# Kernel tuning notes

Hardware: AMD Instinct MI355X
Metric: run time of the kernel (lower is better)

The kernel has to match this reference:

```python
import jax, jax.numpy as jnp
import numpy as np

H = 128        # num_hidden
NIN = 384      # num_in
FF = 4 * H
SCALE = 30.0
EPS = 1e-5


def _gelu(x):
    return jax.nn.gelu(x, approximate=False)


def _layernorm(x, g, b):
    mu = jnp.mean(x, axis=-1, keepdims=True)
    var = jnp.var(x, axis=-1, keepdims=True)
    return (x - mu) * jax.lax.rsqrt(var + EPS) * g + b


def setup_inputs() -> dict:
    key = jax.random.key(0)
    ks = jax.random.split(key, 12)
    B, N, K = 4, 2048, 48
    s = lambda fan_in: 1.0 / np.sqrt(fan_in)
    inp = {
        "h_V": jax.random.normal(ks[0], (B, N, H), jnp.float32),
        "h_E": jax.random.normal(ks[1], (B, N, K, NIN), jnp.float32),
        "mask_V": jnp.ones((B, N), jnp.float32),
        "mask_attend": jnp.ones((B, N, K), jnp.float32),
        "W1_w": jax.random.uniform(ks[2], (H + NIN, H), jnp.float32, -s(H + NIN), s(H + NIN)),
        "W1_b": jnp.zeros((H,), jnp.float32),
        "W2_w": jax.random.uniform(ks[3], (H, H), jnp.float32, -s(H), s(H)),
        "W2_b": jnp.zeros((H,), jnp.float32),
        "W3_w": jax.random.uniform(ks[4], (H, H), jnp.float32, -s(H), s(H)),
        "W3_b": jnp.zeros((H,), jnp.float32),
        "Win_w": jax.random.uniform(ks[5], (H, FF), jnp.float32, -s(H), s(H)),
        "Win_b": jnp.zeros((FF,), jnp.float32),
        "Wout_w": jax.random.uniform(ks[6], (FF, H), jnp.float32, -s(FF), s(FF)),
        "Wout_b": jnp.zeros((H,), jnp.float32),
        "ln1_g": jnp.ones((H,), jnp.float32),
        "ln1_b": jnp.zeros((H,), jnp.float32),
        "ln2_g": jnp.ones((H,), jnp.float32),
        "ln2_b": jnp.zeros((H,), jnp.float32),
    }
    return inp


def reference(h_V, h_E, mask_V, mask_attend,
              W1_w, W1_b, W2_w, W2_b, W3_w, W3_b,
              Win_w, Win_b, Wout_w, Wout_b,
              ln1_g, ln1_b, ln2_g, ln2_b):
    B, N, K, _ = h_E.shape
    # expand node feats over K neighbors and concat with edge feats -> [B,N,K,H+NIN]
    h_V_expand = jnp.broadcast_to(h_V[:, :, None, :], (B, N, K, h_V.shape[-1]))
    h_EV = jnp.concatenate([h_V_expand, h_E], axis=-1)
    # edge MLP: 3 linears, 2 GELUs
    h_message = _gelu(h_EV @ W1_w + W1_b)
    h_message = _gelu(h_message @ W2_w + W2_b)
    h_message = h_message @ W3_w + W3_b
    h_message = mask_attend[..., None] * h_message
    dh = jnp.sum(h_message, axis=-2) / SCALE  # [B,N,H]
    h = _layernorm(h_V + dh, ln1_g, ln1_b)
    # position-wise FFN
    dh = _gelu(h @ Win_w + Win_b) @ Wout_w + Wout_b
    h = _layernorm(h + dh, ln2_g, ln2_b)
    h = mask_V[..., None] * h
    return h
```

## Files before the change

### kernel.cpp

```cpp
#include <hip/hip_runtime.h>
#include <hip/hip_bf16.h>

#define Hh    128
#define NINc  384
#define KN    48
#define FFd   512
#define NNODE 8192
#define NPB   32
#define EGRID (NNODE/NPB)

typedef __attribute__((ext_vector_type(8))) short short8v;
typedef __attribute__((ext_vector_type(4))) float f32x4;

__device__ __forceinline__ short f2bf(float f){
  union { float f; unsigned u; } v; v.f = f;
  unsigned r = v.u + 0x7FFFu + ((v.u >> 16) & 1u);
  return (short)(r >> 16);
}

__device__ __forceinline__ float gelu_f(float x){
  float t = 0.7978845608028654f * x * (1.0f + 0.044715f * x * x);
  float e = __expf(2.0f * t);
  return x * (1.0f - 1.0f / (e + 1.0f));
}

__global__ void prep_weights(const float* __restrict__ W1, const float* __restrict__ W2,
                             const float* __restrict__ W3, const float* __restrict__ Win,
                             const float* __restrict__ Wout,
                             short* __restrict__ w1vT, short* __restrict__ w1eT,
                             short* __restrict__ w2T,  short* __restrict__ w3T,
                             short* __restrict__ winT, short* __restrict__ woutT)
{
  int i = blockIdx.x * 256 + threadIdx.x;
  if (i < 16384){ int n = i / 128, k = i % 128; w1vT[i] = f2bf(W1[k*128 + n]); return; }
  i -= 16384;
  if (i < 49152){ int n = i / 384, k = i % 384; w1eT[i] = f2bf(W1[(128+k)*128 + n]); return; }
  i -= 49152;
  if (i < 16384){ int n = i / 128, k = i % 128; w2T[i] = f2bf(W2[k*128 + n]); return; }
  i -= 16384;
  if (i < 16384){ int n = i / 128, k = i % 128; w3T[i] = f2bf(W3[k*128 + n]); return; }
  i -= 16384;
  if (i < 65536){ int n = i / 128, k = i % 128; winT[i] = f2bf(Win[k*512 + n]); return; }
  i -= 65536;
  if (i < 65536){ int n = i / 512, k = i % 512; woutT[i] = f2bf(Wout[k*128 + n]); return; }
}

__global__ __launch_bounds__(256,2) void np_kernel(
    const float* __restrict__ hV, const short* __restrict__ w1vT,
    const float* __restrict__ b1, float* __restrict__ npart)
{
  const int row0 = blockIdx.x * 64;
  const int tid = threadIdx.x, lane = tid & 63, wv = tid >> 6;
  __shared__ __attribute__((aligned(16))) short Xs[64][Hh + 8];

  const float4* src = (const float4*)(hV + (size_t)row0 * Hh);
  #pragma unroll
  for (int j = 0; j < 8; ++j){
    int idx = tid + 256*j;
    int r = idx >> 5, c4 = idx & 31;
    float4 v = src[idx];
    short4 s = make_short4(f2bf(v.x), f2bf(v.y), f2bf(v.z), f2bf(v.w));
    *(short4*)&Xs[r][c4*4] = s;
  }
  __syncthreads();

  const int arow = lane & 15, kgrp = (lane >> 4) * 8;
  const int col0 = wv * 32, ccol = lane & 15, crow0 = (lane >> 4) * 4;

  f32x4 acc[4][2];
  #pragma unroll
  for (int m = 0; m < 4; ++m) for (int n = 0; n < 2; ++n) acc[m][n] = (f32x4){0.f,0.f,0.f,0.f};

  const short8v* Bw = (const short8v*)w1vT;
  #pragma unroll
  for (int ks = 0; ks < 4; ++ks){
    int kb = ks*32 + kgrp;
    short8v b0 = Bw[(col0 + arow)*16      + (kb >> 3)];
    short8v b1f = Bw[(col0 + 16 + arow)*16 + (kb >> 3)];
    #pragma unroll
    for (int m = 0; m < 4; ++m){
      short8v a = *(const short8v*)&Xs[m*16 + arow][kb];
      acc[m][0] = __builtin_amdgcn_mfma_f32_16x16x32_bf16(a, b0,  acc[m][0], 0,0,0);
      acc[m][1] = __builtin_amdgcn_mfma_f32_16x16x32_bf16(a, b1f, acc[m][1], 0,0,0);
    }
  }
  #pragma unroll
  for (int m = 0; m < 4; ++m) for (int n = 0; n < 2; ++n){
    int colg = col0 + n*16 + ccol;
    float bb = b1[colg];
    #pragma unroll
    for (int r = 0; r < 4; ++r)
      npart[(size_t)(row0 + m*16 + crow0 + r)*Hh + colg] = acc[m][n][r] + bb;
  }
}

__global__ __launch_bounds__(512,2) void edge_kernel(
    const float* __restrict__ hE, const float* __restrict__ hV,
    const float* __restrict__ maskA, const float* __restrict__ npart,
    const short* __restrict__ w1eT, const short* __restrict__ w2T,
    const short* __restrict__ w3T,
    const float* __restrict__ b2, const float* __restrict__ b3,
    float* __restrict__ out)
{
  const int tid = threadIdx.x, lane = tid & 63, wv = tid >> 6;
  const int base = blockIdx.x * NPB;

  __shared__ __attribute__((aligned(16))) short Et[KN][NINc + 8];
  __shared__ __attribute__((aligned(16))) short M1[KN][Hh + 8];
  __shared__ float mskS[KN];
  __shared__ float npS[Hh], hvS[Hh];

  short (*M2)[Hh + 8] = (short (*)[Hh + 8])&Et[0][0];

  const int arow = lane & 15, kgrp = (lane >> 4) * 8;
  const int ccol = lane & 15, crow0 = (lane >> 4) * 4;
  const int col0 = wv * 16;
  const int colg = col0 + ccol;

  short8v w1f[12], w2f[4], w3f[4];
  {
    const short8v* B1 = (const short8v*)w1eT;
    const short8v* B2 = (const short8v*)w2T;
    const short8v* B3 = (const short8v*)w3T;
    const int rB = col0 + arow;
    #pragma unroll
    for (int ks = 0; ks < 12; ++ks) w1f[ks] = B1[rB*48 + ((ks*32 + kgrp) >> 3)];
    #pragma unroll
    for (int ks = 0; ks < 4; ++ks){
      w2f[ks] = B2[rB*16 + ((ks*32 + kgrp) >> 3)];
      w3f[ks] = B3[rB*16 + ((ks*32 + kgrp) >> 3)];
    }
  }
  const float b2v = b2[colg];
  const float b3v = b3[colg];

  float4 pf[9];
  float  pmsk = 0.f;
  float4 phv  = {0,0,0,0}, pnp = {0,0,0,0};

  auto LOADN = [&](int nn){
    const float4* src = (const float4*)(hE + (size_t)nn * (KN*NINc));
    #pragma unroll
    for (int j = 0; j < 4; ++j){
      pf[2*j]   = src[2*tid + 1024*j];
      pf[2*j+1] = src[2*tid + 1024*j + 1];
    }
    pf[8] = src[4096 + tid];
    if (tid < KN) pmsk = maskA[nn*KN + tid];
    if (tid >= 64 && tid < 96)  phv = *(const float4*)(hV    + (size_t)nn*Hh + (tid-64)*4);
    if (tid >= 96 && tid < 128) pnp = *(const float4*)(npart + (size_t)nn*Hh + (tid-96)*4);
  };
  auto STOREN = [&](){
    #pragma unroll
    for (int j = 0; j < 4; ++j){
      int e0 = 2*tid + 1024*j;
      int r = e0 / 96, c = e0 - r*96;
      short8v s8;
      s8[0]=f2bf(pf[2*j].x);   s8[1]=f2bf(pf[2*j].y);
      s8[2]=f2bf(pf[2*j].z);   s8[3]=f2bf(pf[2*j].w);
      s8[4]=f2bf(pf[2*j+1].x); s8[5]=f2bf(pf[2*j+1].y);
      s8[6]=f2bf(pf[2*j+1].z); s8[7]=f2bf(pf[2*j+1].w);
      *(short8v*)&Et[r][c*4] = s8;
    }
    { int e = 4096 + tid; int r = e / 96, c = e - r*96;
      *(short4*)&Et[r][c*4] =
        make_short4(f2bf(pf[8].x), f2bf(pf[8].y), f2bf(pf[8].z), f2bf(pf[8].w)); }
    if (tid < KN) mskS[tid] = pmsk;
    if (tid >= 64 && tid < 96)  *(float4*)&hvS[(tid-64)*4] = phv;
    if (tid >= 96 && tid < 128) *(float4*)&npS[(tid-96)*4] = pnp;
  };

  LOADN(base);
  STOREN();
  __syncthreads();

  for (int t = 0; t < NPB; ++t){
    const int node = base + t;
    if (t + 1 < NPB) LOADN(node + 1);

    {
      f32x4 a1[3];
      #pragma unroll
      for (int m = 0; m < 3; ++m) a1[m] = (f32x4){0.f,0.f,0.f,0.f};
      #pragma unroll
      for (int ks = 0; ks < 12; ++ks){
        int kb = ks*32 + kgrp;
        short8v v0 = *(const short8v*)&Et[arow][kb];
        short8v v1 = *(const short8v*)&Et[16 + arow][kb];
        short8v v2 = *(const short8v*)&Et[32 + arow][kb];
        a1[0] = __builtin_amdgcn_mfma_f32_16x16x32_bf16(v0, w1f[ks], a1[0], 0,0,0);
        a1[1] = __builtin_amdgcn_mfma_f32_16x16x32_bf16(v1, w1f[ks], a1[1], 0,0,0);
        a1[2] = __builtin_amdgcn_mfma_f32_16x16x32_bf16(v2, w1f[ks], a1[2], 0,0,0);
      }
      float npv = npS[colg];
      #pragma unroll
      for (int m = 0; m < 3; ++m)
        #pragma unroll
        for (int r = 0; r < 4; ++r)
          M1[m*16 + crow0 + r][colg] = f2bf(gelu_f(a1[m][r] + npv));
    }
    __syncthreads();

    {
      f32x4 a2[3];
      #pragma unroll
      for (int m = 0; m < 3; ++m) a2[m] = (f32x4){0.f,0.f,0.f,0.f};
      #pragma unroll
      for (int ks = 0; ks < 4; ++ks){
        int kb = ks*32 + kgrp;
        short8v v0 = *(const short8v*)&M1[arow][kb];
        short8v v1 = *(const short8v*)&M1[16 + arow][kb];
        short8v v2 = *(const short8v*)&M1[32 + arow][kb];
        a2[0] = __builtin_amdgcn_mfma_f32_16x16x32_bf16(v0, w2f[ks], a2[0], 0,0,0);
        a2[1] = __builtin_amdgcn_mfma_f32_16x16x32_bf16(v1, w2f[ks], a2[1], 0,0,0);
        a2[2] = __builtin_amdgcn_mfma_f32_16x16x32_bf16(v2, w2f[ks], a2[2], 0,0,0);
      }
      #pragma unroll
      for (int m = 0; m < 3; ++m)
        #pragma unroll
        for (int r = 0; r < 4; ++r)
          M2[m*16 + crow0 + r][colg] = f2bf(gelu_f(a2[m][r] + b2v));
    }
    __syncthreads();

    {
      f32x4 a3[3];
      #pragma unroll
      for (int m = 0; m < 3; ++m) a3[m] = (f32x4){0.f,0.f,0.f,0.f};
      #pragma unroll
      for (int ks = 0; ks < 4; ++ks){
        int kb = ks*32 + kgrp;
        short8v v0 = *(const short8v*)&M2[arow][kb];
        short8v v1 = *(const short8v*)&M2[16 + arow][kb];
        short8v v2 = *(const short8v*)&M2[32 + arow][kb];
        a3[0] = __builtin_amdgcn_mfma_f32_16x16x32_bf16(v0, w3f[ks], a3[0], 0,0,0);
        a3[1] = __builtin_amdgcn_mfma_f32_16x16x32_bf16(v1, w3f[ks], a3[1], 0,0,0);
        a3[2] = __builtin_amdgcn_mfma_f32_16x16x32_bf16(v2, w3f[ks], a3[2], 0,0,0);
      }
      float s = 0.f;
      #pragma unroll
      for (int m = 0; m < 3; ++m)
        #pragma unroll
        for (int r = 0; r < 4; ++r)
          s += (a3[m][r] + b3v) * mskS[m*16 + crow0 + r];
      s += __shfl_xor(s, 16);
      s += __shfl_xor(s, 32);
      if (lane < 16)
        out[(size_t)node*Hh + colg] = hvS[colg] + s * (1.0f/30.0f);
    }
    __syncthreads();

    if (t + 1 < NPB){
      STOREN();
      __syncthreads();
    }
  }
}

__global__ __launch_bounds__(256,2) void ffn_kernel(
    const float* __restrict__ ln1g, const float* __restrict__ ln1b,
    const short* __restrict__ winT, const float* __restrict__ bin,
    const short* __restrict__ woutT, const float* __restrict__ bout,
    const float* __restrict__ ln2g, const float* __restrict__ ln2b,
    const float* __restrict__ maskV, float* __restrict__ io)
{
  const int row0 = blockIdx.x * 32;
  const int tid = threadIdx.x, lane = tid & 63, wv = tid >> 6;
  __shared__ __attribute__((aligned(16))) short Xs[32][Hh + 8];
  __shared__ __attribute__((aligned(16))) float Rs[32][Hh + 4];
  __shared__ __attribute__((aligned(16))) short Hs[32][FFd + 8];

  const int arow = lane & 15, kgrp = (lane >> 4) * 8;
  const int ccol = lane & 15, crow0 = (lane >> 4) * 4;

  {
    int r = tid >> 3, cb = (tid & 7) * 16;
    const float4* xp = (const float4*)(io + (size_t)(row0 + r)*Hh + cb);
    float xv[16];
    #pragma unroll
    for (int j = 0; j < 4; ++j){
      float4 v = xp[j];
      xv[j*4+0]=v.x; xv[j*4+1]=v.y; xv[j*4+2]=v.z; xv[j*4+3]=v.w;
    }
    float sum = 0.f, sq = 0.f;
    #pragma unroll
    for (int j = 0; j < 16; ++j){ sum += xv[j]; sq += xv[j]*xv[j]; }
    #pragma unroll
    for (int d = 1; d < 8; d <<= 1){ sum += __shfl_xor(sum, d); sq += __shfl_xor(sq, d); }
    float mu = sum * (1.0f/128.0f);
    float var = sq * (1.0f/128.0f) - mu*mu;
    float rstd = rsqrtf(var + 1e-5f);
    #pragma unroll
    for (int j = 0; j < 16; ++j){
      int c = cb + j;
      float xn = (xv[j] - mu) * rstd * ln1g[c] + ln1b[c];
      Xs[r][c] = f2bf(xn);
      Rs[r][c] = xn;
    }
  }
  __syncthreads();

  {
    f32x4 acc[2][8];
    #pragma unroll
    for (int m = 0; m < 2; ++m) for (int n = 0; n < 8; ++n) acc[m][n] = (f32x4){0.f,0.f,0.f,0.f};
    const short8v* Bw = (const short8v*)winT;
    #pragma unroll
    for (int ks = 0; ks < 4; ++ks){
      int kb = ks*32 + kgrp;
      short8v a0 = *(const short8v*)&Xs[arow][kb];
      short8v a1 = *(const short8v*)&Xs[16 + arow][kb];
      #pragma unroll
      for (int n = 0; n < 8; ++n){
        short8v b = Bw[(wv*128 + n*16 + arow)*16 + (kb >> 3)];
        acc[0][n] = __builtin_amdgcn_mfma_f32_16x16x32_bf16(a0,b,acc[0][n],0,0,0);
        acc[1][n] = __builtin_amdgcn_mfma_f32_16x16x32_bf16(a1,b,acc[1][n],0,0,0);
      }
    }
    #pragma unroll
    for (int m = 0; m < 2; ++m) for (int n = 0; n < 8; ++n){
      int colg = wv*128 + n*16 + ccol;
      float bb = bin[colg];
      #pragma unroll
      for (int r = 0; r < 4; ++r)
        Hs[m*16 + crow0 + r][colg] = f2bf(gelu_f(acc[m][n][r] + bb));
    }
  }
  __syncthreads();

  {
    f32x4 acc[2][2];
    #pragma unroll
    for (int m = 0; m < 2; ++m) for (int n = 0; n < 2; ++n) acc[m][n] = (f32x4){0.f,0.f,0.f,0.f};
    const short8v* Bw = (const short8v*)woutT;
    #pragma unroll
    for (int ks = 0; ks < 16; ++ks){
      int kb = ks*32 + kgrp;
      short8v a0 = *(const short8v*)&Hs[arow][kb];
      short8v a1 = *(const short8v*)&Hs[16 + arow][kb];
      short8v b0 = Bw[(wv*32 + arow)*64      + (kb >> 3)];
      short8v b1f = Bw[(wv*32 + 16 + arow)*64 + (kb >> 3)];
      acc[0][0] = __builtin_amdgcn_mfma_f32_16x16x32_bf16(a0,b0, acc[0][0],0,0,0);
      acc[1][0] = __builtin_amdgcn_mfma_f32_16x16x32_bf16(a1,b0, acc[1][0],0,0,0);
      acc[0][1] = __builtin_amdgcn_mfma_f32_16x16x32_bf16(a0,b1f,acc[0][1],0,0,0);
      acc[1][1] = __builtin_amdgcn_mfma_f32_16x16x32_bf16(a1,b1f,acc[1][1],0,0,0);
    }
    #pragma unroll
    for (int m = 0; m < 2; ++m) for (int n = 0; n < 2; ++n){
      int colg = wv*32 + n*16 + ccol;
      float bb = bout[colg];
      #pragma unroll
      for (int r = 0; r < 4; ++r){
        int rr = m*16 + crow0 + r;
        Rs[rr][colg] = Rs[rr][colg] + acc[m][n][r] + bb;
      }
    }
  }
  __syncthreads();

  {
    int r = tid >> 3, cb = (tid & 7) * 16;
    float xv[16];
    #pragma unroll
    for (int j = 0; j < 16; ++j) xv[j] = Rs[r][cb + j];
    float sum = 0.f, sq = 0.f;
    #pragma unroll
    for (int j = 0; j < 16; ++j){ sum += xv[j]; sq += xv[j]*xv[j]; }
    #pragma unroll
    for (int d = 1; d < 8; d <<= 1){ sum += __shfl_xor(sum, d); sq += __shfl_xor(sq, d); }
    float mu = sum * (1.0f/128.0f);
    float var = sq * (1.0f/128.0f) - mu*mu;
    float rstd = rsqrtf(var + 1e-5f);
    float mv = maskV[row0 + r];
    float* op = io + (size_t)(row0 + r)*Hh + cb;
    #pragma unroll
    for (int j = 0; j < 4; ++j){
      float4 o;
      o.x = ((xv[j*4+0] - mu)*rstd*ln2g[cb+j*4+0] + ln2b[cb+j*4+0]) * mv;
      o.y = ((xv[j*4+1] - mu)*rstd*ln2g[cb+j*4+1] + ln2b[cb+j*4+1]) * mv;
      o.z = ((xv[j*4+2] - mu)*rstd*ln2g[cb+j*4+2] + ln2b[cb+j*4+2]) * mv;
      o.w = ((xv[j*4+3] - mu)*rstd*ln2g[cb+j*4+3] + ln2b[cb+j*4+3]) * mv;
      ((float4*)op)[j] = o;
    }
  }
}

extern "C" void kernel_launch(void* const* d_in, const int* in_sizes, int n_in,
                              void* d_out, int out_size, void* d_ws, size_t ws_size,
                              hipStream_t stream)
{
  const float* hV    = (const float*)d_in[0];
  const float* hE    = (const float*)d_in[1];
  const float* maskV = (const float*)d_in[2];
  const float* maskA = (const float*)d_in[3];
  const float* W1w   = (const float*)d_in[4];
  const float* W1b   = (const float*)d_in[5];
  const float* W2w   = (const float*)d_in[6];
  const float* W2b   = (const float*)d_in[7];
  const float* W3w   = (const float*)d_in[8];
  const float* W3b   = (const float*)d_in[9];
  const float* Winw  = (const float*)d_in[10];
  const float* Winb  = (const float*)d_in[11];
  const float* Woutw = (const float*)d_in[12];
  const float* Woutb = (const float*)d_in[13];
  const float* l1g   = (const float*)d_in[14];
  const float* l1b   = (const float*)d_in[15];
  const float* l2g   = (const float*)d_in[16];
  const float* l2b   = (const float*)d_in[17];

  char* ws = (char*)d_ws;
  size_t off = 0;
  float* npart = (float*)(ws + off); off += (size_t)NNODE * Hh * 4;
  short* w1vT  = (short*)(ws + off); off += 128*128*2;
  short* w1eT  = (short*)(ws + off); off += 128*384*2;
  short* w2T   = (short*)(ws + off); off += 128*128*2;
  short* w3T   = (short*)(ws + off); off += 128*128*2;
  short* winT  = (short*)(ws + off); off += 512*128*2;
  short* woutT = (short*)(ws + off); off += 128*512*2;
  if (ws_size < off) return;

  prep_weights<<<896, 256, 0, stream>>>(W1w, W2w, W3w, Winw, Woutw,
                                        w1vT, w1eT, w2T, w3T, winT, woutT);
  np_kernel<<<NNODE/64, 256, 0, stream>>>(hV, w1vT, W1b, npart);
  edge_kernel<<<EGRID, 512, 0, stream>>>(hE, hV, maskA, npart,
                                         w1eT, w2T, w3T, W2b, W3b, (float*)d_out);
  ffn_kernel<<<NNODE/32, 256, 0, stream>>>(l1g, l1b, winT, Winb, woutT, Woutb,
                                           l2g, l2b, maskV, (float*)d_out);
}
```

Baseline: 234.4 us.

## Double-buffer edge tile in LDS, use packed bf16 conversion and lighter barriers

The edge kernel now keeps two LDS buffers for the edge tile, mask, h_V and npart. The next node's data is stored into the idle buffer, so one block-wide barrier per node can be dropped, and M2 gets its own array instead of aliasing the edge tile. The manual float-to-bf16 rounding is replaced by the HIP bf16 intrinsics, including a packed two-value conversion. __syncthreads is replaced by an inline-asm wait on lgkmcnt plus s_barrier. The extra LDS (roughly 2x the edge tile) may reduce occupancy below the two blocks per CU requested by the launch bounds, and the hand-written barrier relies on an exact wait-count behaviour.

```diff
diff --git a/kernel.cpp b/kernel.cpp
--- a/kernel.cpp
+++ b/kernel.cpp
@@ -12,16 +12,24 @@
 typedef __attribute__((ext_vector_type(8))) short short8v;
 typedef __attribute__((ext_vector_type(4))) float f32x4;
 
-__device__ __forceinline__ short f2bf(float f){
-  union { float f; unsigned u; } v; v.f = f;
-  unsigned r = v.u + 0x7FFFu + ((v.u >> 16) & 1u);
-  return (short)(r >> 16);
+__device__ __forceinline__ short f2bf1(float f){
+  union { __hip_bfloat16 h; short s; } c; c.h = __float2bfloat16(f);
+  return c.s;
+}
+__device__ __forceinline__ unsigned pk_bf16(float lo, float hi){
+  union { __hip_bfloat162 h; unsigned u; } c;
+  c.h = __float22bfloat162_rn(make_float2(lo, hi));
+  return c.u;
 }
 
 __device__ __forceinline__ float gelu_f(float x){
   float t = 0.7978845608028654f * x * (1.0f + 0.044715f * x * x);
   float e = __expf(2.0f * t);
   return x * (1.0f - 1.0f / (e + 1.0f));
+}
+
+__device__ __forceinline__ void bar_lds(){
+  asm volatile("s_waitcnt lgkmcnt(0)\n\ts_barrier" ::: "memory");
 }
 
 __global__ void prep_weights(const float* __restrict__ W1, const float* __restrict__ W2,
@@ -32,17 +40,17 @@
                              short* __restrict__ winT, short* __restrict__ woutT)
 {
   int i = blockIdx.x * 256 + threadIdx.x;
-  if (i < 16384){ int n = i / 128, k = i % 128; w1vT[i] = f2bf(W1[k*128 + n]); return; }
+  if (i < 16384){ int n = i / 128, k = i % 128; w1vT[i] = f2bf1(W1[k*128 + n]); return; }
   i -= 16384;
-  if (i < 49152){ int n = i / 384, k = i % 384; w1eT[i] = f2bf(W1[(128+k)*128 + n]); return; }
+  if (i < 49152){ int n = i / 384, k = i % 384; w1eT[i] = f2bf1(W1[(128+k)*128 + n]); return; }
   i -= 49152;
-  if (i < 16384){ int n = i / 128, k = i % 128; w2T[i] = f2bf(W2[k*128 + n]); return; }
+  if (i < 16384){ int n = i / 128, k = i % 128; w2T[i] = f2bf1(W2[k*128 + n]); return; }
   i -= 16384;
-  if (i < 16384){ int n = i / 128, k = i % 128; w3T[i] = f2bf(W3[k*128 + n]); return; }
+  if (i < 16384){ int n = i / 128, k = i % 128; w3T[i] = f2bf1(W3[k*128 + n]); return; }
   i -= 16384;
-  if (i < 65536){ int n = i / 128, k = i % 128; winT[i] = f2bf(Win[k*512 + n]); return; }
+  if (i < 65536){ int n = i / 128, k = i % 128; winT[i] = f2bf1(Win[k*512 + n]); return; }
   i -= 65536;
-  if (i < 65536){ int n = i / 512, k = i % 512; woutT[i] = f2bf(Wout[k*128 + n]); return; }
+  if (i < 65536){ int n = i / 512, k = i % 512; woutT[i] = f2bf1(Wout[k*128 + n]); return; }
 }
 
 __global__ __launch_bounds__(256,2) void np_kernel(
@@ -59,8 +67,8 @@
     int idx = tid + 256*j;
     int r = idx >> 5, c4 = idx & 31;
     float4 v = src[idx];
-    short4 s = make_short4(f2bf(v.x), f2bf(v.y), f2bf(v.z), f2bf(v.w));
-    *(short4*)&Xs[r][c4*4] = s;
+    unsigned u0 = pk_bf16(v.x, v.y), u1 = pk_bf16(v.z, v.w);
+    *(uint2*)&Xs[r][c4*4] = make_uint2(u0, u1);
   }
   __syncthreads();
 
@@ -105,12 +113,11 @@
   const int tid = threadIdx.x, lane = tid & 63, wv = tid >> 6;
   const int base = blockIdx.x * NPB;
 
-  __shared__ __attribute__((aligned(16))) short Et[KN][NINc + 8];
+  __shared__ __attribute__((aligned(16))) short Etd[2][KN][NINc + 8];
   __shared__ __attribute__((aligned(16))) short M1[KN][Hh + 8];
-  __shared__ float mskS[KN];
-  __shared__ float npS[Hh], hvS[Hh];
-
-  short (*M2)[Hh + 8] = (short (*)[Hh + 8])&Et[0][0];
+  __shared__ __attribute__((aligned(16))) short M2[KN][Hh + 8];
+  __shared__ float mskS[2][KN];
+  __shared__ float npS[2][Hh], hvS[2][Hh];
 
   const int arow = lane & 15, kgrp = (lane >> 4) * 8;
   const int ccol = lane & 15, crow0 = (lane >> 4) * 4;
@@ -150,30 +157,31 @@
     if (tid >= 64 && tid < 96)  phv = *(const float4*)(hV    + (size_t)nn*Hh + (tid-64)*4);
     if (tid >= 96 && tid < 128) pnp = *(const float4*)(npart + (size_t)nn*Hh + (tid-96)*4);
   };
-  auto STOREN = [&](){
+  auto STOREN = [&](int buf){
     #pragma unroll
     for (int j = 0; j < 4; ++j){
       int e0 = 2*tid + 1024*j;
       int r = e0 / 96, c = e0 - r*96;
-      short8v s8;
-      s8[0]=f2bf(pf[2*j].x);   s8[1]=f2bf(pf[2*j].y);
-      s8[2]=f2bf(pf[2*j].z);   s8[3]=f2bf(pf[2*j].w);
-      s8[4]=f2bf(pf[2*j+1].x); s8[5]=f2bf(pf[2*j+1].y);
-      s8[6]=f2bf(pf[2*j+1].z); s8[7]=f2bf(pf[2*j+1].w);
-      *(short8v*)&Et[r][c*4] = s8;
+      uint4 u;
+      u.x = pk_bf16(pf[2*j].x,   pf[2*j].y);
+      u.y = pk_bf16(pf[2*j].z,   pf[2*j].w);
+      u.z = pk_bf16(pf[2*j+1].x, pf[2*j+1].y);
+      u.w = pk_bf16(pf[2*j+1].z, pf[2*j+1].w);
+      *(uint4*)&Etd[buf][r][c*4] = u;
     }
     { int e = 4096 + tid; int r = e / 96, c = e - r*96;
-      *(short4*)&Et[r][c*4] =
-        make_short4(f2bf(pf[8].x), f2bf(pf[8].y), f2bf(pf[8].z), f2bf(pf[8].w)); }
-    if (tid < KN) mskS[tid] = pmsk;
-    if (tid >= 64 && tid < 96)  *(float4*)&hvS[(tid-64)*4] = phv;
-    if (tid >= 96 && tid < 128) *(float4*)&npS[(tid-96)*4] = pnp;
+      *(uint2*)&Etd[buf][r][c*4] =
+        make_uint2(pk_bf16(pf[8].x, pf[8].y), pk_bf16(pf[8].z, pf[8].w)); }
+    if (tid < KN) mskS[buf][tid] = pmsk;
+    if (tid >= 64 && tid < 96)  *(float4*)&hvS[buf][(tid-64)*4] = phv;
+    if (tid >= 96 && tid < 128) *(float4*)&npS[buf][(tid-96)*4] = pnp;
   };
 
   LOADN(base);
-  STOREN();
-  __syncthreads();
-
+  STOREN(0);
+  bar_lds();
+
+  int cur = 0;
   for (int t = 0; t < NPB; ++t){
     const int node = base + t;
     if (t + 1 < NPB) LOADN(node + 1);
@@ -185,21 +193,21 @@
       #pragma unroll
       for (int ks = 0; ks < 12; ++ks){
         int kb = ks*32 + kgrp;
-        short8v v0 = *(const short8v*)&Et[arow][kb];
-        short8v v1 = *(const short8v*)&Et[16 + arow][kb];
-        short8v v2 = *(const short8v*)&Et[32 + arow][kb];
+        short8v v0 = *(const short8v*)&Etd[cur][arow][kb];
+        short8v v1 = *(const short8v*)&Etd[cur][16 + arow][kb];
+        short8v v2 = *(const short8v*)&Etd[cur][32 + arow][kb];
         a1[0] = __builtin_amdgcn_mfma_f32_16x16x32_bf16(v0, w1f[ks], a1[0], 0,0,0);
         a1[1] = __builtin_amdgcn_mfma_f32_16x16x32_bf16(v1, w1f[ks], a1[1], 0,0,0);
         a1[2] = __builtin_amdgcn_mfma_f32_16x16x32_bf16(v2, w1f[ks], a1[2], 0,0,0);
       }
-      float npv = npS[colg];
+      float npv = npS[cur][colg];
       #pragma unroll
       for (int m = 0; m < 3; ++m)
         #pragma unroll
         for (int r = 0; r < 4; ++r)
-          M1[m*16 + crow0 + r][colg] = f2bf(gelu_f(a1[m][r] + npv));
-    }
-    __syncthreads();
+          M1[m*16 + crow0 + r][colg] = f2bf1(gelu_f(a1[m][r] + npv));
+    }
+    bar_lds();
 
     {
       f32x4 a2[3];
@@ -219,9 +227,9 @@
       for (int m = 0; m < 3; ++m)
         #pragma unroll
         for (int r = 0; r < 4; ++r)
-          M2[m*16 + crow0 + r][colg] = f2bf(gelu_f(a2[m][r] + b2v));
-    }
-    __syncthreads();
+          M2[m*16 + crow0 + r][colg] = f2bf1(gelu_f(a2[m][r] + b2v));
+    }
+    bar_lds();
 
     {
       f32x4 a3[3];
@@ -242,18 +250,18 @@
       for (int m = 0; m < 3; ++m)
         #pragma unroll
         for (int r = 0; r < 4; ++r)
-          s += (a3[m][r] + b3v) * mskS[m*16 + crow0 + r];
+          s += (a3[m][r] + b3v) * mskS[cur][m*16 + crow0 + r];
       s += __shfl_xor(s, 16);
       s += __shfl_xor(s, 32);
       if (lane < 16)
-        out[(size_t)node*Hh + colg] = hvS[colg] + s * (1.0f/30.0f);
-    }
-    __syncthreads();
+        out[(size_t)node*Hh + colg] = hvS[cur][colg] + s * (1.0f/30.0f);
+    }
 
     if (t + 1 < NPB){
-      STOREN();
-      __syncthreads();
-    }
+      STOREN(cur ^ 1);
+      bar_lds();
+    }
+    cur ^= 1;
   }
 }
 
@@ -294,7 +302,7 @@
     for (int j = 0; j < 16; ++j){
       int c = cb + j;
       float xn = (xv[j] - mu) * rstd * ln1g[c] + ln1b[c];
-      Xs[r][c] = f2bf(xn);
+      Xs[r][c] = f2bf1(xn);
       Rs[r][c] = xn;
     }
   }
@@ -323,7 +331,7 @@
       float bb = bin[colg];
       #pragma unroll
       for (int r = 0; r < 4; ++r)
-        Hs[m*16 + crow0 + r][colg] = f2bf(gelu_f(acc[m][n][r] + bb));
+        Hs[m*16 + crow0 + r][colg] = f2bf1(gelu_f(acc[m][n][r] + bb));
     }
   }
   __syncthreads();
```

Measured after the change: 225.6 us. 3.8% less time.
